# Optimization experiments

Measured on AMD Instinct MI355X. Metric: run time of the kernel, lower is better.

Reference implementation:

```python
import jax, jax.numpy as jnp
import numpy as np

IN_FEATURES = 4096
OUT_FEATURES = 11008
BATCH, SEQ = 4, 2048


def setup_inputs() -> dict:
    key = jax.random.key(0)
    k1, k2, k3 = jax.random.split(key, 3)
    x = jax.random.normal(k1, (BATCH, SEQ, IN_FEATURES), dtype=jnp.float32)
    # int8-valued weights stored as int32 (values in [-128, 127])
    weight_int8 = jax.random.randint(k2, (OUT_FEATURES, IN_FEATURES), -128, 128, dtype=jnp.int32)
    # per-output-channel positive scales, typical magnitude ~ max|w|/127
    scale = jax.random.uniform(k3, (OUT_FEATURES,), dtype=jnp.float32, minval=1e-4, maxval=0.05)
    return {"x": x, "weight_int8": weight_int8, "scale": scale}


def reference(x, weight_int8, scale):
    # Dequantize: per-channel symmetric, weight[o, i] = int8[o, i] * scale[o]
    weight = weight_int8.astype(x.dtype) * scale.astype(x.dtype)[:, None]
    # F.linear: x @ weight.T  -> [B, S, out_features]
    return jnp.einsum("bsi,oi->bso", x, weight)
```

## Files before the change

kernel.cpp:

```cpp
#include <hip/hip_runtime.h>
#include <hip/hip_bf16.h>


#define M_DIM 8192
#define N_DIM 11008
#define K_DIM 4096

#define BM 256
#define BN 256
#define BK 128

using f32x4  = __attribute__((ext_vector_type(4))) float;
using i32x4  = __attribute__((ext_vector_type(4))) int;
using s16x4  = __attribute__((ext_vector_type(4))) short;
using s16x8  = __attribute__((ext_vector_type(8))) short;

typedef __attribute__((address_space(3))) void lds_void_t;
typedef __attribute__((address_space(1))) const void gbl_void_t;

__device__ __forceinline__ short cvt_bf16(float f) {
    union { float f; unsigned u; } v; v.f = f;
    unsigned r = v.u + 0x7fffu + ((v.u >> 16) & 1u);
    return (short)(r >> 16);
}

__global__ __launch_bounds__(256) void quant_x(const float* __restrict__ X,
                                               signed char* __restrict__ Q,
                                               float* __restrict__ sx) {
    const int row = blockIdx.x;
    const int tid = threadIdx.x;
    const f32x4* xr = (const f32x4*)(X + (size_t)row * K_DIM);

    f32x4 v[4];
    float m = 0.f;
    #pragma unroll
    for (int i = 0; i < 4; ++i) {
        v[i] = xr[tid * 4 + i];
        #pragma unroll
        for (int j = 0; j < 4; ++j) m = fmaxf(m, fabsf(v[i][j]));
    }
    #pragma unroll
    for (int off = 32; off; off >>= 1) m = fmaxf(m, __shfl_xor(m, off));
    __shared__ float wmax[4];
    if ((tid & 63) == 0) wmax[tid >> 6] = m;
    __syncthreads();
    m = fmaxf(fmaxf(wmax[0], wmax[1]), fmaxf(wmax[2], wmax[3]));

    const float inv = (m > 0.f) ? 127.0f / m : 0.f;
    i32x4 o;
    #pragma unroll
    for (int i = 0; i < 4; ++i) {
        int b0 = __float2int_rn(v[i][0] * inv) & 255;
        int b1 = __float2int_rn(v[i][1] * inv) & 255;
        int b2 = __float2int_rn(v[i][2] * inv) & 255;
        int b3 = __float2int_rn(v[i][3] * inv) & 255;
        o[i] = b0 | (b1 << 8) | (b2 << 16) | (b3 << 24);
    }
    ((i32x4*)(Q + (size_t)row * K_DIM))[tid] = o;
    if (tid == 0) sx[row] = (m > 0.f) ? m * (1.0f / 127.0f) : 0.f;
}

__global__ __launch_bounds__(256) void convert_w(const int* __restrict__ W,
                                                 signed char* __restrict__ Q, int n16) {
    int i = blockIdx.x * blockDim.x + threadIdx.x;
    const int stride = gridDim.x * blockDim.x;
    for (; i < n16; i += stride) {
        i32x4 o;
        #pragma unroll
        for (int j = 0; j < 4; ++j) {
            i32x4 v = ((const i32x4*)W)[i * 4 + j];
            o[j] = (v[0] & 255) | ((v[1] & 255) << 8) | ((v[2] & 255) << 16) | (v[3] << 24);
        }
        ((i32x4*)Q)[i] = o;
    }
}

#define SBAR __builtin_amdgcn_s_barrier()
#define LGKM(n) do { asm volatile("s_waitcnt lgkmcnt(" #n ")" ::: "memory"); \
                     __builtin_amdgcn_sched_barrier(0); } while (0)
#define WAIT_VM(n) do { asm volatile("s_waitcnt vmcnt(" #n ")" ::: "memory"); \
                        __builtin_amdgcn_sched_barrier(0); } while (0)

#define STAGE(bufi, opi, srcp, T) do {                                             \
    signed char* _d = &lds[bufi][opi][0];                                          \
    const size_t _toff = (size_t)((T) & 31) * 128;                                 \
    _Pragma("unroll")                                                              \
    for (int _i = 0; _i < 4; ++_i)                                                 \
        __builtin_amdgcn_global_load_lds(                                          \
            (gbl_void_t*)((srcp) + (size_t)_i * 64 * K_DIM + _toff),               \
            (lds_void_t*)(_d + (_i * 512 + tid) * 16), 16, 0, 0);                  \
} while (0)

#define READ_A(dst, bufi, qm) do {                                                 \
    const signed char* _s = &lds[bufi][0][0];                                      \
    _Pragma("unroll")                                                              \
    for (int _m = 0; _m < 4; ++_m)                                                 \
        _Pragma("unroll")                                                          \
        for (int _k = 0; _k < 2; ++_k)                                             \
            dst[_m][_k] = *(const i32x4*)(_s                                       \
                + (size_t)((mi * 128 + (qm) * 64 + _m * 16 + fr) * 128)            \
                + ((((_k << 2) | fq) ^ fr7) << 4));                                \
} while (0)

#define READ_B(dst, bufi, qn) do {                                                 \
    const signed char* _s = &lds[bufi][1][0];                                      \
    _Pragma("unroll")                                                              \
    for (int _n = 0; _n < 2; ++_n)                                                 \
        _Pragma("unroll")                                                          \
        for (int _k = 0; _k < 2; ++_k)                                             \
            dst[_n][_k] = *(const i32x4*)(_s                                       \
                + (size_t)((ni * 64 + (qn) * 32 + _n * 16 + fr) * 128)             \
                + ((((_k << 2) | fq) ^ fr7) << 4));                                \
} while (0)

#define MFMA_Q(qm, qn, aset, bset) do {                                            \
    __builtin_amdgcn_s_setprio(1);                                                 \
    _Pragma("unroll")                                                              \
    for (int _m = 0; _m < 4; ++_m)                                                 \
        _Pragma("unroll")                                                          \
        for (int _n = 0; _n < 2; ++_n)                                             \
            _Pragma("unroll")                                                      \
            for (int _k = 0; _k < 2; ++_k)                                         \
                acc[(qm) * 4 + _m][(qn) * 2 + _n] =                                \
                    __builtin_amdgcn_mfma_i32_16x16x64_i8(                         \
                        aset[_m][_k], bset[_n][_k],                                \
                        acc[(qm) * 4 + _m][(qn) * 2 + _n], 0, 0, 0);               \
    __builtin_amdgcn_s_setprio(0);                                                 \
} while (0)

#define HALF_ITER(BUF, T) do {                                                     \
                                                                     \
    READ_A(a0, BUF, 0);                                                            \
    READ_B(b0, BUF, 0);                                                            \
    SBAR; LGKM(0);                                                                 \
    MFMA_Q(0, 0, a0, b0);                                                          \
    SBAR;                                                                          \
                                                                     \
    READ_B(b1, BUF, 1);                                                            \
    SBAR; LGKM(0);                                                                 \
    MFMA_Q(0, 1, a0, b1);                                                          \
    SBAR;                                                                          \
                                                      \
    READ_A(a1, BUF, 1);                                                            \
    STAGE(BUF, 1, Bsrc, (T) + 2);                                                  \
    SBAR; LGKM(0);                                                                 \
    MFMA_Q(1, 1, a1, b1);                                                          \
    SBAR;                                                                          \
                             \
    STAGE(BUF, 0, Asrc, (T) + 2);                                                  \
    WAIT_VM(8);                                                                    \
    SBAR;                                                                          \
    MFMA_Q(1, 0, a1, b0);                                                          \
    SBAR;                                                                          \
} while (0)

__global__ __launch_bounds__(512, 2) void gemm_i8(
    const signed char* __restrict__ A,
    const signed char* __restrict__ B,
    const float* __restrict__ sx,
    const float* __restrict__ scale,
    float*       __restrict__ C)
{
    __shared__ __align__(16) signed char lds[2][2][256 * 128];

    const int tid  = threadIdx.x;
    const int lane = tid & 63;
    const int fr   = lane & 15;
    const int fq   = lane >> 4;
    const int fr7  = fr & 7;
    const int wave = tid >> 6;
    const int mi   = wave >> 2;
    const int ni   = wave & 3;

    const int bid = blockIdx.x;
    const int xcd = bid & 7;
    const int idx = bid >> 3;
    const int bm  = xcd * 4 + (idx & 3);
    const int bn  = idx >> 2;

    const int jl   = (tid & 7) ^ ((tid >> 3) & 7);
    const int soff = (tid >> 3) * K_DIM + jl * 16;
    const signed char* Asrc = A + (size_t)bm * BM * K_DIM + soff;
    const signed char* Bsrc = B + (size_t)bn * BN * K_DIM + soff;

    i32x4 acc[8][4] = {};
    i32x4 a0[4][2], a1[4][2], b0[2][2], b1[2][2];

    STAGE(0, 1, Bsrc, 0);
    STAGE(0, 0, Asrc, 0);
    STAGE(1, 1, Bsrc, 1);
    STAGE(1, 0, Asrc, 1);
    WAIT_VM(8);
    SBAR;

    for (int it = 0; it < 16; ++it) {
        const int t0 = 2 * it;
        HALF_ITER(0, t0);
        HALF_ITER(1, t0 + 1);
    }

    const int row0 = bm * BM + mi * 128 + fq * 4;
    const int col0 = bn * BN + ni * 64 + fr;
    float s4[4];
    #pragma unroll
    for (int jn = 0; jn < 4; ++jn) s4[jn] = scale[col0 + jn * 16];
    #pragma unroll
    for (int i = 0; i < 8; ++i) {
        #pragma unroll
        for (int jj = 0; jj < 4; ++jj) {
            const int r = row0 + i * 16 + jj;
            const float sxv = sx[r];
            #pragma unroll
            for (int jn = 0; jn < 4; ++jn)
                __builtin_nontemporal_store(
                    (float)acc[i][jn][jj] * sxv * s4[jn],
                    &C[(size_t)r * N_DIM + col0 + jn * 16]);
        }
    }
}

#define FBM 128
#define FBN 128
#define FBK 32
#define LDK 40
__global__ __launch_bounds__(256) void int8_linear_fused(
    const float* __restrict__ A, const int* __restrict__ W,
    const float* __restrict__ scale, float* __restrict__ C)
{
    __shared__ short As[FBM][LDK];
    __shared__ short Bs[FBN][LDK];
    const int tid = threadIdx.x;
    const int bid = blockIdx.x;
    const int g   = bid / (8 * 86);
    const int rem = bid % (8 * 86);
    const int bm  = g * 8 + (rem & 7);
    const int bn  = rem >> 3;
    const int srow = tid >> 3;
    const int skq  = tid & 7;
    const float* Ab = A + (size_t)(bm * FBM + srow) * K_DIM + skq * 4;
    const int*   Wb = W + (size_t)(bn * FBN + srow) * K_DIM + skq * 4;
    const int lane = tid & 63, wave = tid >> 6;
    const int wm = (wave >> 1) * 64, wn = (wave & 1) * 64;
    const int fr = lane & 15, fq = lane >> 4;
    f32x4 acc[4][4] = {};
    f32x4 areg[4]; i32x4 breg[4];
    #pragma unroll
    for (int i = 0; i < 4; ++i) {
        areg[i] = *(const f32x4*)(Ab + (size_t)(i * 32) * K_DIM);
        breg[i] = *(const i32x4*)(Wb + (size_t)(i * 32) * K_DIM);
    }
    const int NT = K_DIM / FBK;
    for (int kt = 0; kt < NT; ++kt) {
        __syncthreads();
        #pragma unroll
        for (int i = 0; i < 4; ++i) {
            s16x4 av, bv;
            #pragma unroll
            for (int j = 0; j < 4; ++j) {
                av[j] = cvt_bf16(areg[i][j]);
                bv[j] = cvt_bf16((float)breg[i][j]);
            }
            *(s16x4*)&As[srow + i * 32][skq * 4] = av;
            *(s16x4*)&Bs[srow + i * 32][skq * 4] = bv;
        }
        __syncthreads();
        if (kt + 1 < NT) {
            const int k0 = (kt + 1) * FBK;
            #pragma unroll
            for (int i = 0; i < 4; ++i) {
                areg[i] = *(const f32x4*)(Ab + (size_t)(i * 32) * K_DIM + k0);
                breg[i] = *(const i32x4*)(Wb + (size_t)(i * 32) * K_DIM + k0);
            }
        }
        s16x8 af[4], bf[4];
        #pragma unroll
        for (int m = 0; m < 4; ++m) af[m] = *(const s16x8*)&As[wm + m * 16 + fr][fq * 8];
        #pragma unroll
        for (int n = 0; n < 4; ++n) bf[n] = *(const s16x8*)&Bs[wn + n * 16 + fr][fq * 8];
        #pragma unroll
        for (int m = 0; m < 4; ++m)
            #pragma unroll
            for (int n = 0; n < 4; ++n)
                acc[m][n] = __builtin_amdgcn_mfma_f32_16x16x32_bf16(af[m], bf[n], acc[m][n], 0, 0, 0);
    }
    #pragma unroll
    for (int n = 0; n < 4; ++n) {
        const int gn = bn * FBN + wn + n * 16 + fr;
        const float s = scale[gn];
        #pragma unroll
        for (int m = 0; m < 4; ++m) {
            const int gm0 = bm * FBM + wm + m * 16 + fq * 4;
            #pragma unroll
            for (int j = 0; j < 4; ++j)
                C[(size_t)(gm0 + j) * N_DIM + gn] = acc[m][n][j] * s;
        }
    }
}

extern "C" void kernel_launch(void* const* d_in, const int* in_sizes, int n_in,
                              void* d_out, int out_size, void* d_ws, size_t ws_size,
                              hipStream_t stream) {
    const float* x  = (const float*)d_in[0];
    const int*   w  = (const int*)d_in[1];
    const float* sc = (const float*)d_in[2];
    float* out = (float*)d_out;

    const size_t w_bytes  = (size_t)N_DIM * K_DIM;
    const size_t x_bytes  = (size_t)M_DIM * K_DIM;
    const size_t sx_bytes = (size_t)M_DIM * sizeof(float);
    const size_t need = w_bytes + x_bytes + sx_bytes;

    if (ws_size >= need) {
        signed char* qw = (signed char*)d_ws;
        signed char* qx = qw + w_bytes;
        float* sx = (float*)(qx + x_bytes);
        convert_w<<<dim3(2048), dim3(256), 0, stream>>>(w, qw, (int)(w_bytes / 16));
        quant_x<<<dim3(M_DIM), dim3(256), 0, stream>>>(x, qx, sx);
        const int nblocks = (M_DIM / BM) * (N_DIM / BN);
        gemm_i8<<<dim3(nblocks), dim3(512), 0, stream>>>(qx, qw, sx, sc, out);
    } else {
        const int nblocks = (M_DIM / FBM) * (N_DIM / FBN);
        int8_linear_fused<<<dim3(nblocks), dim3(256), 0, stream>>>(x, w, sc, out);
    }
}
```

Before: 434.5 us.

## Load A fragments directly from global into registers, stage only B in LDS

Removes LDS staging for the activation operand A. Each wave now reads its MFMA A fragments straight from global memory into registers, one K-step ahead. Only B is double-buffered through LDS, which halves LDS footprint and removes the LDS write/read round trip and several barriers for A. The cost is that every A fragment is fetched from global/L2 by all four column waves, which raises cache traffic. It also makes completion of the B LDS DMA depend on implicit vmcnt waits, and it adds register pressure.

After: 1.046 ms. +140.8%, slower.

```diff
diff --git a/kernel.cpp b/kernel.cpp
--- a/kernel.cpp
+++ b/kernel.cpp
@@ -81,8 +81,8 @@
 #define WAIT_VM(n) do { asm volatile("s_waitcnt vmcnt(" #n ")" ::: "memory"); \
                         __builtin_amdgcn_sched_barrier(0); } while (0)
 
-#define STAGE(bufi, opi, srcp, T) do {                                             \
-    signed char* _d = &lds[bufi][opi][0];                                          \
+#define STAGE(bufi, srcp, T) do {                                                  \
+    signed char* _d = &lds[bufi][0];                                               \
     const size_t _toff = (size_t)((T) & 31) * 128;                                 \
     _Pragma("unroll")                                                              \
     for (int _i = 0; _i < 4; ++_i)                                                 \
@@ -91,19 +91,18 @@
             (lds_void_t*)(_d + (_i * 512 + tid) * 16), 16, 0, 0);                  \
 } while (0)
 
-#define READ_A(dst, bufi, qm) do {                                                 \
-    const signed char* _s = &lds[bufi][0][0];                                      \
+#define READ_AG(dst, qm, T) do {                                                   \
     _Pragma("unroll")                                                              \
     for (int _m = 0; _m < 4; ++_m)                                                 \
         _Pragma("unroll")                                                          \
         for (int _k = 0; _k < 2; ++_k)                                             \
-            dst[_m][_k] = *(const i32x4*)(_s                                       \
-                + (size_t)((mi * 128 + (qm) * 64 + _m * 16 + fr) * 128)            \
-                + ((((_k << 2) | fq) ^ fr7) << 4));                                \
+            dst[_m][_k] = *(const i32x4*)(Afrag                                    \
+                + (size_t)((qm) * 64 + _m * 16) * K_DIM                            \
+                + (size_t)(T) * 128 + (_k << 6));                                  \
 } while (0)
 
 #define READ_B(dst, bufi, qn) do {                                                 \
-    const signed char* _s = &lds[bufi][1][0];                                      \
+    const signed char* _s = &lds[bufi][0];                                         \
     _Pragma("unroll")                                                              \
     for (int _n = 0; _n < 2; ++_n)                                                 \
         _Pragma("unroll")                                                          \
@@ -129,29 +128,24 @@
 } while (0)
 
 #define HALF_ITER(BUF, T) do {                                                     \
-                                                                     \
-    READ_A(a0, BUF, 0);                                                            \
+                                                           \
     READ_B(b0, BUF, 0);                                                            \
-    SBAR; LGKM(0);                                                                 \
-    MFMA_Q(0, 0, a0, b0);                                                          \
+    READ_B(b1, BUF, 1);                                                            \
+    LGKM(4);                                                                       \
+    MFMA_Q(0, 0, aF0, b0);                                                         \
+    LGKM(0);                                                                       \
     SBAR;                                                                          \
-                                                                     \
-    READ_B(b1, BUF, 1);                                                            \
-    SBAR; LGKM(0);                                                                 \
-    MFMA_Q(0, 1, a0, b1);                                                          \
+                               \
+    READ_AG(aF1, 1, (T));                                                          \
+    STAGE(BUF, Bsrc, (T) + 2);                                                     \
+    MFMA_Q(0, 1, aF0, b1);                                                         \
     SBAR;                                                                          \
-                                                      \
-    READ_A(a1, BUF, 1);                                                            \
-    STAGE(BUF, 1, Bsrc, (T) + 2);                                                  \
-    SBAR; LGKM(0);                                                                 \
-    MFMA_Q(1, 1, a1, b1);                                                          \
+                                           \
+    READ_AG(aF0, 0, (T) + 1);                                                      \
+    MFMA_Q(1, 1, aF1, b1);                                                         \
     SBAR;                                                                          \
-                             \
-    STAGE(BUF, 0, Asrc, (T) + 2);                                                  \
-    WAIT_VM(8);                                                                    \
-    SBAR;                                                                          \
-    MFMA_Q(1, 0, a1, b0);                                                          \
-    SBAR;                                                                          \
+                                               \
+    MFMA_Q(1, 0, aF1, b0);                                                         \
 } while (0)
 
 __global__ __launch_bounds__(512, 2) void gemm_i8(
@@ -161,7 +155,7 @@
     const float* __restrict__ scale,
     float*       __restrict__ C)
 {
-    __shared__ __align__(16) signed char lds[2][2][256 * 128];
+    __shared__ __align__(16) signed char lds[2][256 * 128];
 
     const int tid  = threadIdx.x;
     const int lane = tid & 63;
@@ -180,23 +174,23 @@
 
     const int jl   = (tid & 7) ^ ((tid >> 3) & 7);
     const int soff = (tid >> 3) * K_DIM + jl * 16;
-    const signed char* Asrc = A + (size_t)bm * BM * K_DIM + soff;
     const signed char* Bsrc = B + (size_t)bn * BN * K_DIM + soff;
 
+    const signed char* Afrag = A + (size_t)(bm * BM + mi * 128 + fr) * K_DIM + fq * 16;
+
     i32x4 acc[8][4] = {};
-    i32x4 a0[4][2], a1[4][2], b0[2][2], b1[2][2];
-
-    STAGE(0, 1, Bsrc, 0);
-    STAGE(0, 0, Asrc, 0);
-    STAGE(1, 1, Bsrc, 1);
-    STAGE(1, 0, Asrc, 1);
-    WAIT_VM(8);
+    i32x4 aF0[4][2], aF1[4][2];
+    i32x4 b0[2][2], b1[2][2];
+
+    STAGE(0, Bsrc, 0);
+    STAGE(1, Bsrc, 1);
+    READ_AG(aF0, 0, 0);
+    WAIT_VM(12);
     SBAR;
 
     for (int it = 0; it < 16; ++it) {
-        const int t0 = 2 * it;
-        HALF_ITER(0, t0);
-        HALF_ITER(1, t0 + 1);
+        HALF_ITER(0, 2 * it);
+        HALF_ITER(1, 2 * it + 1);
     }
 
     const int row0 = bm * BM + mi * 128 + fq * 4;
```
